# Kernel optimization log

Measured on AMD Instinct MI355X. Metric: run time of the kernel, lower is better.

The kernel has to match this reference:

```python
import jax, jax.numpy as jnp
import numpy as np

B, H, W = 16, 32, 64
HID, VOCAB, ENC_C, EMB = 256, 5000, 1024, 256


def _conv3x3(x, w, b):
    # x: [B,C,H,W], w: [O,I,3,3]
    y = jax.lax.conv_general_dilated(x, w, (1, 1), 'SAME',
                                     dimension_numbers=('NCHW', 'OIHW', 'NCHW'))
    return y + b[None, :, None, None]


def _gru(x, h, w_ih, w_hh, b_ih, b_hh):
    # torch GRUCell: gates ordered r, z, n
    gi = x @ w_ih.T + b_ih
    gh = h @ w_hh.T + b_hh
    ir, iz, inn = jnp.split(gi, 3, axis=1)
    hr, hz, hn = jnp.split(gh, 3, axis=1)
    r = jax.nn.sigmoid(ir + hr)
    z = jax.nn.sigmoid(iz + hz)
    n = jnp.tanh(inn + r * hn)
    return (1.0 - z) * n + z * h


def setup_inputs() -> dict:
    key = jax.random.key(0)
    ks = jax.random.split(key, 48)
    g = lambda i, shape, s=0.02: jax.random.normal(ks[i], shape, jnp.float32) * s
    inp = {
        'input_a': jax.random.randint(ks[0], (B,), 0, VOCAB),
        'input_hidden': jax.random.normal(ks[1], (B, 1, HID), jnp.float32),
        'encoder_outputs': jax.random.normal(ks[2], (B, ENC_C, H, W), jnp.float32),
        'attention_sum': jnp.zeros((B, 1, H, W), jnp.float32),
        'decoder_attention': jnp.zeros((B, 1, H, W), jnp.float32),
        'h_mask': jax.random.randint(ks[3], (B,), 1, H + 1),
        'w_mask': jax.random.randint(ks[4], (B,), 1, W + 1),
        'feature_w': W, 'feature_h': H, 'batch_size': B, 'gpu': 0,
        # parameters
        'emb_w': g(5, (VOCAB, EMB)),
        'gru1_w_ih': g(6, (3 * HID, EMB)), 'gru1_w_hh': g(7, (3 * HID, HID)),
        'gru1_b_ih': jnp.zeros((3 * HID,)), 'gru1_b_hh': jnp.zeros((3 * HID,)),
        'fc1_w': g(8, (256, HID)), 'fc1_b': jnp.zeros((256,)),
        'gru2_w_ih': g(9, (3 * HID, ENC_C)), 'gru2_w_hh': g(10, (3 * HID, HID)),
        'gru2_b_ih': jnp.zeros((3 * HID,)), 'gru2_b_hh': jnp.zeros((3 * HID,)),
        'out_w': g(11, (VOCAB, 128)), 'out_b': jnp.zeros((VOCAB,)),
        'emb2_w': g(12, (128, 256)), 'emb2_b': jnp.zeros((128,)),
        'conv1_w': g(13, (1, 1, 3, 3)), 'conv1_b': jnp.zeros((1,)),
        'convtan_w': g(14, (256, 256, 3, 3)), 'convtan_b': jnp.zeros((256,)),
        'fc2_w': g(15, (128, HID)), 'fc2_b': jnp.zeros((128,)),
        'ua_w': g(16, (256, ENC_C)), 'ua_b': jnp.zeros((256,)),
        'uf_w': g(17, (256, 1)), 'uf_b': jnp.zeros((256,)),
        'v_w': g(18, (1, 256)), 'v_b': jnp.zeros((1,)),
        'wc_w': g(19, (128, ENC_C)), 'wc_b': jnp.zeros((128,)),
        'bn1_g': jnp.ones((256,)), 'bn1_b': jnp.zeros((256,)),
        'bn1_rm': jnp.zeros((256,)), 'bn1_rv': jnp.ones((256,)),
    }
    return inp


def reference(input_a, input_hidden, encoder_outputs, feature_w, attention_sum,
              decoder_attention, feature_h, batch_size, h_mask, w_mask, gpu,
              emb_w, gru1_w_ih, gru1_w_hh, gru1_b_ih, gru1_b_hh, fc1_w, fc1_b,
              gru2_w_ih, gru2_w_hh, gru2_b_ih, gru2_b_hh, out_w, out_b,
              emb2_w, emb2_b, conv1_w, conv1_b, convtan_w, convtan_b,
              fc2_w, fc2_b, ua_w, ua_b, uf_w, uf_b, v_w, v_b, wc_w, wc_b,
              bn1_g, bn1_b, bn1_rm, bn1_rv):
    # vectorized mask construction (replaces per-batch python loop)
    mask = ((jnp.arange(feature_h)[None, :, None] < h_mask[:, None, None]) &
            (jnp.arange(feature_w)[None, None, :] < w_mask[:, None, None])
            ).astype(jnp.float32)  # [B,H,W]

    emb = emb_w[input_a]                                   # [B,256] (dropout=eval id)
    h0 = input_hidden.reshape(batch_size, HID)
    st = _gru(emb, h0, gru1_w_ih, gru1_w_hh, gru1_b_ih, gru1_b_hh)  # [B,HID]
    hidden1 = (st @ fc1_w.T + fc1_b)[:, None, None, :]     # [B,1,1,256]

    enc_t = jnp.transpose(encoder_outputs, (0, 2, 3, 1))   # [B,H,W,1024]
    dec_att = _conv3x3(decoder_attention, conv1_w, conv1_b)
    att_sum = attention_sum + dec_att                      # [B,1,H,W]
    att_t = jnp.transpose(att_sum, (0, 2, 3, 1))           # [B,H,W,1]

    enc1 = enc_t @ ua_w.T + ua_b                           # [B,H,W,256]
    att1 = att_t @ uf_w.T + uf_b                           # [B,H,W,256]
    et = hidden1 + enc1 + att1

    et_c = jnp.transpose(et, (0, 3, 1, 2))                 # [B,256,H,W]
    et_c = _conv3x3(et_c, convtan_w, convtan_b)
    et_c = et_c * mask[:, None]
    inv_std = (bn1_g / jnp.sqrt(bn1_rv + 1e-5))[None, :, None, None]
    et_c = (et_c - bn1_rm[None, :, None, None]) * inv_std + bn1_b[None, :, None, None]
    et_c = jnp.tanh(et_c)
    et_hw = jnp.transpose(et_c, (0, 2, 3, 1))              # [B,H,W,256]

    e = (et_hw @ v_w.T + v_b)[..., 0]                      # [B,H,W]
    e_exp = jnp.exp(e) * mask
    e_sum = e_exp.sum((1, 2))                              # [B]
    alpha = e_exp / (e_sum[:, None, None] + 1e-8)
    alpha4 = alpha[:, None]                                # [B,1,H,W]

    ct = (alpha4 * encoder_outputs).sum((2, 3))            # [B,1024]
    h2 = _gru(ct, st, gru2_w_ih, gru2_w_hh, gru2_b_ih, gru2_b_hh)
    hidden_next = h2[:, None, :]                           # [B,1,HID]

    pre = (h2 @ fc2_w.T + fc2_b) + (emb @ emb2_w.T + emb2_b) + (ct @ wc_w.T + wc_b)
    output = jax.nn.log_softmax(pre @ out_w.T + out_b, axis=1)[:, None, :]  # [B,1,V]
    return (output, hidden_next, alpha4, att_sum)
```

## Files before the change

kernel.cpp:

```cpp
#include <hip/hip_runtime.h>
#include <hip/hip_bf16.h>

#define HH 32
#define WW 64
#define HWSZ 2048
#define ENC 1024
#define VOCAB 5000

typedef __attribute__((ext_vector_type(8))) short short8;
typedef __attribute__((ext_vector_type(4))) short short4v;
typedef __attribute__((ext_vector_type(4))) float f32x4;

#if defined(__has_builtin)
#if __has_builtin(__builtin_amdgcn_global_load_lds)
#define HAVE_GLD_LDS 1
#endif
#endif

__device__ __forceinline__ float sigm(float x) { return 1.0f / (1.0f + expf(-x)); }

__device__ __forceinline__ unsigned short f2bf(float x) {
    unsigned u = __float_as_uint(x);
    unsigned r = (u + 0x7fff + ((u >> 16) & 1)) >> 16;
    return (unsigned short)r;
}

#ifdef HAVE_GLD_LDS
__device__ __forceinline__ void gld_lds16(const unsigned short* g, unsigned short* l) {
    __builtin_amdgcn_global_load_lds(
        (const __attribute__((address_space(1))) void*)g,
        (__attribute__((address_space(3))) void*)l,
        16, 0, 0);
}
#endif

template <int NI>
__device__ __forceinline__ float dotk(const float* __restrict__ w,
                                      const float* __restrict__ x, int l) {
    float s = 0.f;
    #pragma unroll
    for (int i = 0; i < NI; ++i) {
        f32x4 wv = *(const f32x4*)(w + i * 64 + l * 4);
        f32x4 xv = *(const f32x4*)(x + i * 64 + l * 4);
        s += wv.x * xv.x + wv.y * xv.y + wv.z * xv.z + wv.w * xv.w;
    }
    return s;
}
__device__ __forceinline__ float red16(float s) {
    s += __shfl_xor(s, 1, 64);
    s += __shfl_xor(s, 2, 64);
    s += __shfl_xor(s, 4, 64);
    s += __shfl_xor(s, 8, 64);
    return s;
}

__global__ __launch_bounds__(256) void k_prep(
    const float* __restrict__ ua_w, unsigned short* __restrict__ ub,
    const float* __restrict__ cw, unsigned short* __restrict__ wr,
    const float* __restrict__ att_in, const float* __restrict__ dec,
    const float* __restrict__ c1w, const float* __restrict__ c1b,
    float* __restrict__ out_attsum,
    const float* __restrict__ wb, const float* __restrict__ g,
    const float* __restrict__ bb, const float* __restrict__ rm,
    const float* __restrict__ rv, float* __restrict__ cs, float* __restrict__ csh,
    const int* __restrict__ input_a, const float* __restrict__ input_hidden,
    const float* __restrict__ emb_w,
    const float* __restrict__ w_ih, const float* __restrict__ w_hh,
    const float* __restrict__ b_ih, const float* __restrict__ b_hh,
    float* __restrict__ gi, float* __restrict__ gh,
    float* __restrict__ e_zero)
{
    int blk = blockIdx.x, t = threadIdx.x;
    if (blk < 1024) {
        int idx = blk * 256 + t;
        ub[idx] = f2bf(ua_w[idx]);
    } else if (blk < 1280) {
        int idx = (blk - 1024) * 256 + t;
        const float* p = cw + (size_t)idx * 9;
        #pragma unroll
        for (int k = 0; k < 9; ++k) wr[k * 65536 + idx] = f2bf(p[k]);
    } else if (blk < 1408) {
        int idx = (blk - 1280) * 256 + t;
        int b = idx >> 11, hw = idx & 2047;
        int h = hw >> 6, w = hw & 63;
        float s = c1b[0];
        #pragma unroll
        for (int dy = 0; dy < 3; ++dy) {
            int hh = h + dy - 1;
            if ((unsigned)hh < (unsigned)HH) {
                #pragma unroll
                for (int dx = 0; dx < 3; ++dx) {
                    int wi = w + dx - 1;
                    if ((unsigned)wi < (unsigned)WW)
                        s += dec[b * HWSZ + hh * WW + wi] * c1w[dy * 3 + dx];
                }
            }
        }
        out_attsum[idx] = att_in[idx] + s;
    } else if (blk == 1408) {
        int c = t;
        float s = g[c] * rsqrtf(rv[c] + 1e-5f);
        cs[c] = s;
        csh[c] = (wb[c] - rm[c]) * s + bb[c];
    } else if (blk < 2177) {
        int gid = (blk - 1409) * 256 + t;
        int o = gid >> 4, l = gid & 15;
        int j = o >> 4, b = o & 15;
        int ia = input_a[b];
        float si = dotk<4>(w_ih + (size_t)j * 256, emb_w + (size_t)ia * 256, l);
        float sh = dotk<4>(w_hh + (size_t)j * 256, input_hidden + b * 256, l);
        si = red16(si); sh = red16(sh);
        if (l == 0) {
            gi[j * 16 + b] = si + b_ih[j];
            gh[j * 16 + b] = sh + b_hh[j];
        }
    } else {
        e_zero[(blk - 2177) * 256 + t] = 0.f;
    }
}

__global__ __launch_bounds__(256) void k_frontbc(
    const int* __restrict__ input_a, const float* __restrict__ emb_w,
    const float* __restrict__ input_hidden,
    const float* __restrict__ gi, const float* __restrict__ gh,
    const float* __restrict__ fc1_w, const float* __restrict__ fc1_b,
    const float* __restrict__ ua_b, const float* __restrict__ uf_b,
    float* __restrict__ st, float* __restrict__ embv, float* __restrict__ addc)
{
    __shared__ float st_s[256];
    int b = blockIdx.x, i = threadIdx.x;
    float r = sigm(gi[i * 16 + b] + gh[i * 16 + b]);
    float z = sigm(gi[(256 + i) * 16 + b] + gh[(256 + i) * 16 + b]);
    float n = tanhf(gi[(512 + i) * 16 + b] + r * gh[(512 + i) * 16 + b]);
    float h0 = input_hidden[b * 256 + i];
    float v = (1.f - z) * n + z * h0;
    st_s[i] = v;
    st[b * 256 + i] = v;
    embv[b * 256 + i] = emb_w[(size_t)input_a[b] * 256 + i];
    __syncthreads();
    int c = i;
    const float* w = fc1_w + (size_t)c * 256;
    float acc = 0.f;
    for (int k = 0; k < 256; ++k) acc += st_s[k] * w[k];
    addc[b * 256 + c] = acc + fc1_b[c] + ua_b[c] + uf_b[c];
}

__global__ __launch_bounds__(256) void k_et(
    const float* __restrict__ enc, const unsigned short* __restrict__ ua_bf,
    const float* __restrict__ addc, const float* __restrict__ uf_w,
    const float* __restrict__ attsum, unsigned short* __restrict__ et)
{
    __shared__ __align__(16) unsigned short As[256 * 64];
    __shared__ __align__(16) unsigned short Bs[32 * 64];
    int t = threadIdx.x;
    int hw0 = blockIdx.x * 32, b = blockIdx.y;
    int wv = t >> 6;
    int l15 = t & 15, quad = (t >> 4) & 3;
    int xb = l15 & 7;
    f32x4 acc[4][2];
    #pragma unroll
    for (int i = 0; i < 4; ++i)
        #pragma unroll
        for (int j = 0; j < 2; ++j) acc[i][j] = (f32x4)0.f;

    int p = t & 31, g3 = t >> 5;
    const float* encb = enc + (size_t)b * ENC * HWSZ + hw0 + p;

    float pfv[8];
    {
        const float* ep = encb + (size_t)(g3 * 8) * HWSZ;
        #pragma unroll
        for (int j = 0; j < 8; ++j) pfv[j] = ep[(size_t)j * HWSZ];
    }

    for (int k0 = 0; k0 < ENC; k0 += 64) {
        short8 bv;
        #pragma unroll
        for (int j = 0; j < 8; ++j) bv[j] = (short)f2bf(pfv[j]);
        if (k0 + 64 < ENC) {
            const float* ep = encb + (size_t)(k0 + 64 + g3 * 8) * HWSZ;
            #pragma unroll
            for (int j = 0; j < 8; ++j) pfv[j] = ep[(size_t)j * HWSZ];
        }
        __syncthreads();

        #pragma unroll
        for (int i = 0; i < 8; ++i) {
            int s = t + 256 * i;
            int c = s >> 3, kq = s & 7;
            const unsigned short* src =
                ua_bf + (size_t)c * ENC + k0 + ((kq ^ (c & 7)) << 3);
#ifdef HAVE_GLD_LDS
            gld_lds16(src, As + (size_t)(wv * 64 + 256 * i) * 8);
#else
            *(uint4*)(As + (size_t)s * 8) = *(const uint4*)src;
#endif
        }
        *(short8*)(Bs + p * 64 + ((g3 ^ (p & 7)) << 3)) = bv;
        __syncthreads();

        #pragma unroll
        for (int kk = 0; kk < 2; ++kk) {
            short8 af[4], bfr[2];
            #pragma unroll
            for (int mt = 0; mt < 4; ++mt) {
                int c = wv * 64 + mt * 16 + l15;
                af[mt] = *(const short8*)(As + c * 64 + (((kk * 4 + quad) ^ xb) << 3));
            }
            #pragma unroll
            for (int nt = 0; nt < 2; ++nt) {
                int n = nt * 16 + l15;
                bfr[nt] = *(const short8*)(Bs + n * 64 + (((kk * 4 + quad) ^ xb) << 3));
            }
            #pragma unroll
            for (int mt = 0; mt < 4; ++mt)
                #pragma unroll
                for (int nt = 0; nt < 2; ++nt)
                    acc[mt][nt] = __builtin_amdgcn_mfma_f32_16x16x32_bf16(
                        af[mt], bfr[nt], acc[mt][nt], 0, 0, 0);
        }
    }
    float at[2];
    #pragma unroll
    for (int nt = 0; nt < 2; ++nt) at[nt] = attsum[b * HWSZ + hw0 + nt * 16 + l15];
    #pragma unroll
    for (int mt = 0; mt < 4; ++mt) {
        int cb = wv * 64 + mt * 16 + quad * 4;
        float ad[4], uw[4];
        #pragma unroll
        for (int r = 0; r < 4; ++r) { ad[r] = addc[b * 256 + cb + r]; uw[r] = uf_w[cb + r]; }
        #pragma unroll
        for (int nt = 0; nt < 2; ++nt) {
            ushort4 pk;
            pk.x = f2bf(acc[mt][nt][0] + ad[0] + at[nt] * uw[0]);
            pk.y = f2bf(acc[mt][nt][1] + ad[1] + at[nt] * uw[1]);
            pk.z = f2bf(acc[mt][nt][2] + ad[2] + at[nt] * uw[2]);
            pk.w = f2bf(acc[mt][nt][3] + ad[3] + at[nt] * uw[3]);
            *(ushort4*)(et + (size_t)(b * HWSZ + hw0 + nt * 16 + l15) * 256 + cb) = pk;
        }
    }
}

__global__ __launch_bounds__(256) void k_conv(
    const unsigned short* __restrict__ et, const unsigned short* __restrict__ wr,
    const float* __restrict__ cs, const float* __restrict__ csh,
    const float* __restrict__ v_w, float* __restrict__ e_out)
{
    __shared__ unsigned short Ls[66 * 264];
    __shared__ float red[64][17];
    int t = threadIdx.x;
    int h = blockIdx.x, c0 = blockIdx.y * 128, b = blockIdx.z;
    int wv = t >> 6, l15 = t & 15, quad = (t >> 4) & 3;
    f32x4 acc[2][4];
    #pragma unroll
    for (int i = 0; i < 2; ++i)
        #pragma unroll
        for (int j = 0; j < 4; ++j) acc[i][j] = (f32x4)0.f;

    for (int dy = 0; dy < 3; ++dy) {
        int hr = h + dy - 1;
        if ((unsigned)hr >= (unsigned)HH) continue;
        __syncthreads();
        const unsigned short* rowp = et + (size_t)(b * HH + hr) * WW * 256;
        for (int idx = t; idx < 2112; idx += 256) {
            int p = idx >> 5, s = idx & 31;
            short8 v;
            if (p == 0 || p == 65) v = (short8)0;
            else v = *(const short8*)(rowp + (p - 1) * 256 + s * 8);
            *(short8*)(Ls + p * 264 + s * 8) = v;
        }
        __syncthreads();
        for (int dx = 0; dx < 3; ++dx) {
            int tap = dy * 3 + dx;
            const unsigned short* wrt = wr + (size_t)tap * 65536;
            #pragma unroll
            for (int kc = 0; kc < 8; ++kc) {
                short8 af[2], bfr[4];
                #pragma unroll
                for (int mt = 0; mt < 2; ++mt)
                    af[mt] = *(const short8*)(wrt +
                        (size_t)(c0 + wv * 32 + mt * 16 + l15) * 256 + kc * 32 + quad * 8);
                #pragma unroll
                for (int nt = 0; nt < 4; ++nt) {
                    int wrow = nt * 16 + l15 + dx;
                    bfr[nt] = *(const short8*)(Ls + wrow * 264 + kc * 32 + quad * 8);
                }
                #pragma unroll
                for (int mt = 0; mt < 2; ++mt)
                    #pragma unroll
                    for (int nt = 0; nt < 4; ++nt)
                        acc[mt][nt] = __builtin_amdgcn_mfma_f32_16x16x32_bf16(
                            af[mt], bfr[nt], acc[mt][nt], 0, 0, 0);
            }
        }
    }
    float p[4] = {0.f, 0.f, 0.f, 0.f};
    #pragma unroll
    for (int mt = 0; mt < 2; ++mt) {
        int cb = c0 + wv * 32 + mt * 16 + quad * 4;
        #pragma unroll
        for (int r = 0; r < 4; ++r) {
            float sc = cs[cb + r], sh = csh[cb + r], vw = v_w[cb + r];
            #pragma unroll
            for (int nt = 0; nt < 4; ++nt) {
                float x = acc[mt][nt][r] * sc + sh;
                p[nt] += tanhf(x) * vw;
            }
        }
    }
    __syncthreads();
    #pragma unroll
    for (int nt = 0; nt < 4; ++nt) red[nt * 16 + l15][wv * 4 + quad] = p[nt];
    __syncthreads();
    if (t < 64) {
        float s = 0.f;
        #pragma unroll
        for (int i = 0; i < 16; ++i) s += red[t][i];
        atomicAdd(&e_out[(b * HH + h) * WW + t], s);
    }
}

__global__ __launch_bounds__(256) void k_ctalpha(
    const float* __restrict__ enc, const float* __restrict__ e_acc,
    const float* __restrict__ v_b,
    const int* __restrict__ h_mask, const int* __restrict__ w_mask,
    float* __restrict__ alpha_out, float* __restrict__ ct)
{
    __shared__ float a_s[HWSZ];
    __shared__ float rbuf[4];
    int b = blockIdx.y, cg = blockIdx.x, t = threadIdx.x;
    int hm = h_mask[b], wm = w_mask[b];
    float vb = v_b[0];
    float vals[8];
    float psum = 0.f;
    #pragma unroll
    for (int u = 0; u < 8; ++u) {
        int s = u * 256 + t;
        int h = s >> 6, w = s & 63;
        float e = e_acc[b * HWSZ + s] + vb;
        float ex = (h < hm && w < wm) ? expf(e) : 0.f;
        vals[u] = ex;
        psum += ex;
    }
    for (int off = 1; off < 64; off <<= 1) psum += __shfl_xor(psum, off, 64);
    if ((t & 63) == 0) rbuf[t >> 6] = psum;
    __syncthreads();
    float inv = 1.f / (rbuf[0] + rbuf[1] + rbuf[2] + rbuf[3] + 1e-8f);
    #pragma unroll
    for (int u = 0; u < 8; ++u) {
        int s = u * 256 + t;
        float a = vals[u] * inv;
        a_s[s] = a;
        if (cg == 0) alpha_out[b * HWSZ + s] = a;
    }
    __syncthreads();
    int wave = t >> 6, lane = t & 63;
    int c = cg * 4 + wave;
    const float* ep = enc + ((size_t)(b * ENC + c)) * HWSZ;
    float s = 0.f;
    for (int i = lane; i < HWSZ; i += 64) s += ep[i] * a_s[i];
    for (int off = 32; off; off >>= 1) s += __shfl_down(s, off, 64);
    if (lane == 0) ct[b * ENC + c] = s;
}

__global__ __launch_bounds__(256) void k_gru2a(
    const float* __restrict__ ct, const float* __restrict__ st,
    const float* __restrict__ w_ih, const float* __restrict__ w_hh,
    const float* __restrict__ b_ih, const float* __restrict__ b_hh,
    float* __restrict__ gi, float* __restrict__ gh)
{
    int gid = blockIdx.x * 256 + threadIdx.x;
    int o = gid >> 4, l = gid & 15;
    int j = o >> 4, b = o & 15;
    float si = dotk<16>(w_ih + (size_t)j * ENC, ct + b * ENC, l);
    float sh = dotk<4>(w_hh + (size_t)j * 256, st + b * 256, l);
    si = red16(si); sh = red16(sh);
    if (l == 0) {
        gi[j * 16 + b] = si + b_ih[j];
        gh[j * 16 + b] = sh + b_hh[j];
    }
}

__global__ __launch_bounds__(256) void k_gates2(
    const float* __restrict__ st, const float* __restrict__ gi,
    const float* __restrict__ gh, float* __restrict__ h2,
    float* __restrict__ out_hidden)
{
    int b = blockIdx.x, i = threadIdx.x;
    float r = sigm(gi[i * 16 + b] + gh[i * 16 + b]);
    float z = sigm(gi[(256 + i) * 16 + b] + gh[(256 + i) * 16 + b]);
    float n = tanhf(gi[(512 + i) * 16 + b] + r * gh[(512 + i) * 16 + b]);
    float v = (1.f - z) * n + z * st[b * 256 + i];
    h2[b * 256 + i] = v;
    out_hidden[b * 256 + i] = v;
}

__global__ __launch_bounds__(256) void k_pre(
    const float* __restrict__ h2, const float* __restrict__ emb,
    const float* __restrict__ ct,
    const float* __restrict__ fc2_w, const float* __restrict__ fc2_b,
    const float* __restrict__ emb2_w, const float* __restrict__ emb2_b,
    const float* __restrict__ wc_w, const float* __restrict__ wc_b,
    float* __restrict__ pre)
{
    int gid = blockIdx.x * 256 + threadIdx.x;
    int o = gid >> 4, l = gid & 15;
    int j = o >> 4, b = o & 15;
    float s = dotk<4>(fc2_w + (size_t)j * 256, h2 + b * 256, l)
            + dotk<4>(emb2_w + (size_t)j * 256, emb + b * 256, l)
            + dotk<16>(wc_w + (size_t)j * ENC, ct + b * ENC, l);
    s = red16(s);
    if (l == 0) pre[b * 128 + j] = s + fc2_b[j] + emb2_b[j] + wc_b[j];
}

__global__ __launch_bounds__(256) void k_logits(
    const float* __restrict__ pre, const float* __restrict__ out_w,
    const float* __restrict__ out_b, float* __restrict__ logits)
{
    int gid = blockIdx.x * 256 + threadIdx.x;
    int o = gid >> 4, l = gid & 15;
    int j = o >> 4, b = o & 15;
    float s = dotk<2>(out_w + (size_t)j * 128, pre + b * 128, l);
    s = red16(s);
    if (l == 0) logits[b * VOCAB + j] = s + out_b[j];
}

__global__ __launch_bounds__(256) void k_lsm(
    const float* __restrict__ logits, float* __restrict__ out)
{
    __shared__ float buf[VOCAB];
    __shared__ float rbuf[4];
    int b = blockIdx.x, t = threadIdx.x;
    float mx = -1e30f;
    for (int s = t; s < VOCAB; s += 256) {
        float v = logits[b * VOCAB + s];
        buf[s] = v;
        mx = fmaxf(mx, v);
    }
    for (int off = 1; off < 64; off <<= 1) mx = fmaxf(mx, __shfl_xor(mx, off, 64));
    if ((t & 63) == 0) rbuf[t >> 6] = mx;
    __syncthreads();
    mx = fmaxf(fmaxf(rbuf[0], rbuf[1]), fmaxf(rbuf[2], rbuf[3]));
    __syncthreads();
    float se = 0.f;
    for (int s = t; s < VOCAB; s += 256) se += expf(buf[s] - mx);
    for (int off = 1; off < 64; off <<= 1) se += __shfl_xor(se, off, 64);
    if ((t & 63) == 0) rbuf[t >> 6] = se;
    __syncthreads();
    float lse = mx + logf(rbuf[0] + rbuf[1] + rbuf[2] + rbuf[3]);
    for (int s = t; s < VOCAB; s += 256) out[b * VOCAB + s] = buf[s] - lse;
}

extern "C" void kernel_launch(void* const* d_in, const int* in_sizes, int n_in,
                              void* d_out, int out_size, void* d_ws, size_t ws_size,
                              hipStream_t stream)
{
    const int*   input_a      = (const int*)d_in[0];
    const float* input_hidden = (const float*)d_in[1];
    const float* enc          = (const float*)d_in[2];
    const float* att_in       = (const float*)d_in[3];
    const float* dec_att      = (const float*)d_in[4];
    const int*   h_mask       = (const int*)d_in[5];
    const int*   w_mask       = (const int*)d_in[6];
    const float* emb_w        = (const float*)d_in[11];
    const float* g1_wih       = (const float*)d_in[12];
    const float* g1_whh       = (const float*)d_in[13];
    const float* g1_bih       = (const float*)d_in[14];
    const float* g1_bhh       = (const float*)d_in[15];
    const float* fc1_w        = (const float*)d_in[16];
    const float* fc1_b        = (const float*)d_in[17];
    const float* g2_wih       = (const float*)d_in[18];
    const float* g2_whh       = (const float*)d_in[19];
    const float* g2_bih       = (const float*)d_in[20];
    const float* g2_bhh       = (const float*)d_in[21];
    const float* out_w        = (const float*)d_in[22];
    const float* out_b        = (const float*)d_in[23];
    const float* emb2_w       = (const float*)d_in[24];
    const float* emb2_b       = (const float*)d_in[25];
    const float* c1w          = (const float*)d_in[26];
    const float* c1b          = (const float*)d_in[27];
    const float* ctw          = (const float*)d_in[28];
    const float* ctb          = (const float*)d_in[29];
    const float* fc2_w        = (const float*)d_in[30];
    const float* fc2_b        = (const float*)d_in[31];
    const float* ua_w         = (const float*)d_in[32];
    const float* ua_b         = (const float*)d_in[33];
    const float* uf_w         = (const float*)d_in[34];
    const float* uf_b         = (const float*)d_in[35];
    const float* v_w          = (const float*)d_in[36];
    const float* v_b          = (const float*)d_in[37];
    const float* wc_w         = (const float*)d_in[38];
    const float* wc_b         = (const float*)d_in[39];
    const float* bn_g         = (const float*)d_in[40];
    const float* bn_b         = (const float*)d_in[41];
    const float* bn_rm        = (const float*)d_in[42];
    const float* bn_rv        = (const float*)d_in[43];

    float* out        = (float*)d_out;
    float* out_logits = out;
    float* out_hidden = out + 80000;
    float* out_alpha  = out + 84096;
    float* out_attsum = out + 116864;

    char* ws = (char*)d_ws;
    unsigned short* et_t  = (unsigned short*)ws;
    unsigned short* ua_bf = (unsigned short*)(ws + 16777216);
    unsigned short* w_r   = (unsigned short*)(ws + 17301504);
    float* f      = (float*)(ws + 18481152);
    float* st     = f;
    float* embv   = f + 4096;
    float* addc   = f + 8192;
    float* e_ws   = f + 12288;
    float* ct     = f + 45056;
    float* h2     = f + 61440;
    float* pre    = f + 65536;
    float* logits = f + 67584;
    float* gi1    = f + 147584;
    float* gh1    = f + 159872;
    float* gi2    = f + 172160;
    float* gh2    = f + 184448;
    float* cs     = f + 196736;
    float* csh    = f + 196992;

    k_prep<<<2305, 256, 0, stream>>>(ua_w, ua_bf, ctw, w_r,
                                     att_in, dec_att, c1w, c1b, out_attsum,
                                     ctb, bn_g, bn_b, bn_rm, bn_rv, cs, csh,
                                     input_a, input_hidden, emb_w,
                                     g1_wih, g1_whh, g1_bih, g1_bhh, gi1, gh1,
                                     e_ws);
    k_frontbc<<<16, 256, 0, stream>>>(input_a, emb_w, input_hidden, gi1, gh1,
                                      fc1_w, fc1_b, ua_b, uf_b, st, embv, addc);

    k_et<<<dim3(64, 16), 256, 0, stream>>>(enc, ua_bf, addc, uf_w, out_attsum, et_t);
    k_conv<<<dim3(32, 2, 16), 256, 0, stream>>>(et_t, w_r, cs, csh, v_w, e_ws);

    k_ctalpha<<<dim3(256, 16), 256, 0, stream>>>(enc, e_ws, v_b, h_mask, w_mask,
                                                 out_alpha, ct);
    k_gru2a<<<768, 256, 0, stream>>>(ct, st, g2_wih, g2_whh, g2_bih, g2_bhh, gi2, gh2);
    k_gates2<<<16, 256, 0, stream>>>(st, gi2, gh2, h2, out_hidden);
    k_pre<<<128, 256, 0, stream>>>(h2, embv, ct, fc2_w, fc2_b, emb2_w, emb2_b,
                                   wc_w, wc_b, pre);
    k_logits<<<5000, 256, 0, stream>>>(pre, out_w, out_b, logits);
    k_lsm<<<16, 256, 0, stream>>>(logits, out_logits);
}
```

Before: 452.0 us.

## Double-buffer conv input rows in LDS with async loads and XOR swizzle

Splits each 3x3 conv input row into two channel halves and stages them into double-buffered LDS using direct global-to-LDS loads, prefetching the next half-row while MFMAs consume the current one. The LDS layout switches from padded rows to an XOR swizzle, and a shared zero buffer stands in for the explicit border columns. It also adds an occupancy hint to launch bounds and raises wave priority around the MFMA section. The aim is to hide global load latency and cut LDS bank conflicts, at the cost of more syncs and extra address arithmetic.

```diff
diff --git a/kernel.cpp b/kernel.cpp
--- a/kernel.cpp
+++ b/kernel.cpp
@@ -241,13 +241,14 @@
     }
 }
 
-__global__ __launch_bounds__(256) void k_conv(
+__global__ __launch_bounds__(256, 4) void k_conv(
     const unsigned short* __restrict__ et, const unsigned short* __restrict__ wr,
     const float* __restrict__ cs, const float* __restrict__ csh,
     const float* __restrict__ v_w, float* __restrict__ e_out)
 {
-    __shared__ unsigned short Ls[66 * 264];
+    __shared__ __align__(16) unsigned short Lh[2 * 8192 + 128];
     __shared__ float red[64][17];
+    unsigned short* Zp = Lh + 16384;
     int t = threadIdx.x;
     int h = blockIdx.x, c0 = blockIdx.y * 128, b = blockIdx.z;
     int wv = t >> 6, l15 = t & 15, quad = (t >> 4) & 3;
@@ -257,33 +258,60 @@
         #pragma unroll
         for (int j = 0; j < 4; ++j) acc[i][j] = (f32x4)0.f;
 
-    for (int dy = 0; dy < 3; ++dy) {
-        int hr = h + dy - 1;
-        if ((unsigned)hr >= (unsigned)HH) continue;
-        __syncthreads();
-        const unsigned short* rowp = et + (size_t)(b * HH + hr) * WW * 256;
-        for (int idx = t; idx < 2112; idx += 256) {
-            int p = idx >> 5, s = idx & 31;
-            short8 v;
-            if (p == 0 || p == 65) v = (short8)0;
-            else v = *(const short8*)(rowp + (p - 1) * 256 + s * 8);
-            *(short8*)(Ls + p * 264 + s * 8) = v;
-        }
-        __syncthreads();
+    if (t < 16) *(short8*)(Zp + t * 8) = (short8)0;
+
+    int ni = 6, ibase = 0;
+    if (h == 0)           { ni = 4; ibase = 2; }
+    else if (h == HH - 1) { ni = 4; }
+
+    const unsigned short* etb = et + (size_t)b * HH * WW * 256;
+
+    auto stage = [&](int item, int bufsel) {
+        int dy = item >> 1, half = item & 1;
+        const unsigned short* rowp = etb + (size_t)(h + dy - 1) * WW * 256 + half * 128;
+        unsigned short* buf = Lh + bufsel * 8192;
+        #pragma unroll
+        for (int j = 0; j < 4; ++j) {
+            int s = t + 256 * j;
+            int r = s >> 4, o = s & 15;
+            const unsigned short* src = rowp + r * 256 + ((o ^ (r & 15)) << 3);
+#ifdef HAVE_GLD_LDS
+            gld_lds16(src, buf + (size_t)(wv * 64 + 256 * j) * 8);
+#else
+            *(uint4*)(buf + (size_t)s * 8) = *(const uint4*)src;
+#endif
+        }
+    };
+
+    stage(ibase, 0);
+    __syncthreads();
+
+    for (int i = 0; i < ni; ++i) {
+        if (i + 1 < ni) stage(ibase + i + 1, (i + 1) & 1);
+
+        int item = ibase + i;
+        int dy = item >> 1, half = item & 1;
+        const unsigned short* buf = Lh + (i & 1) * 8192;
+        __builtin_amdgcn_s_setprio(1);
+        #pragma unroll
         for (int dx = 0; dx < 3; ++dx) {
-            int tap = dy * 3 + dx;
-            const unsigned short* wrt = wr + (size_t)tap * 65536;
+            const unsigned short* wrt =
+                wr + (size_t)(dy * 3 + dx) * 65536 + half * 128;
             #pragma unroll
-            for (int kc = 0; kc < 8; ++kc) {
+            for (int kcl = 0; kcl < 4; ++kcl) {
                 short8 af[2], bfr[4];
                 #pragma unroll
                 for (int mt = 0; mt < 2; ++mt)
                     af[mt] = *(const short8*)(wrt +
-                        (size_t)(c0 + wv * 32 + mt * 16 + l15) * 256 + kc * 32 + quad * 8);
+                        (size_t)(c0 + wv * 32 + mt * 16 + l15) * 256 + kcl * 32 + quad * 8);
+                int o = kcl * 4 + quad;
                 #pragma unroll
                 for (int nt = 0; nt < 4; ++nt) {
-                    int wrow = nt * 16 + l15 + dx;
-                    bfr[nt] = *(const short8*)(Ls + wrow * 264 + kc * 32 + quad * 8);
+                    int r = nt * 16 + l15 + dx - 1;
+                    const unsigned short* p = ((unsigned)r < (unsigned)WW)
+                        ? buf + r * 128 + ((o ^ (r & 15)) << 3)
+                        : Zp + o * 8;
+                    bfr[nt] = *(const short8*)p;
                 }
                 #pragma unroll
                 for (int mt = 0; mt < 2; ++mt)
@@ -293,7 +321,10 @@
                             af[mt], bfr[nt], acc[mt][nt], 0, 0, 0);
             }
         }
-    }
+        __builtin_amdgcn_s_setprio(0);
+        __syncthreads();
+    }
+
     float p[4] = {0.f, 0.f, 0.f, 0.f};
     #pragma unroll
     for (int mt = 0; mt < 2; ++mt) {
```

Result: no change. 448.1 us (-0.9%).

## Double-buffer conv input rows and merge channel halves into one block

Applied to the files above, without the earlier changes.

The 3x3 conv kernel now computes all 256 output channels per block instead of splitting them across two blocks, so each input row is staged into LDS once rather than twice. The e-scores can then be written directly instead of accumulated with atomics. Input rows are prefetched into registers and written into a second LDS buffer while MFMAs run on the current one, with raised priority during the compute phase. The cost is twice as many accumulators per thread and half as many blocks (512), which reduces parallelism and puts pressure on registers. Since e_ws is still zeroed by the prep kernel, storing instead of adding gives the same values.

```diff
diff --git a/kernel.cpp b/kernel.cpp
--- a/kernel.cpp
+++ b/kernel.cpp
@@ -241,63 +241,94 @@
     }
 }
 
-__global__ __launch_bounds__(256) void k_conv(
+__global__ __launch_bounds__(256, 2) void k_conv(
     const unsigned short* __restrict__ et, const unsigned short* __restrict__ wr,
     const float* __restrict__ cs, const float* __restrict__ csh,
     const float* __restrict__ v_w, float* __restrict__ e_out)
 {
-    __shared__ unsigned short Ls[66 * 264];
+    __shared__ __align__(16) unsigned short Ls[2][66 * 264];
     __shared__ float red[64][17];
     int t = threadIdx.x;
-    int h = blockIdx.x, c0 = blockIdx.y * 128, b = blockIdx.z;
+    int h = blockIdx.x, b = blockIdx.y;
     int wv = t >> 6, l15 = t & 15, quad = (t >> 4) & 3;
-    f32x4 acc[2][4];
-    #pragma unroll
-    for (int i = 0; i < 2; ++i)
+    f32x4 acc[4][4];
+    #pragma unroll
+    for (int i = 0; i < 4; ++i)
         #pragma unroll
         for (int j = 0; j < 4; ++j) acc[i][j] = (f32x4)0.f;
 
-    for (int dy = 0; dy < 3; ++dy) {
-        int hr = h + dy - 1;
-        if ((unsigned)hr >= (unsigned)HH) continue;
-        __syncthreads();
-        const unsigned short* rowp = et + (size_t)(b * HH + hr) * WW * 256;
-        for (int idx = t; idx < 2112; idx += 256) {
-            int p = idx >> 5, s = idx & 31;
-            short8 v;
-            if (p == 0 || p == 65) v = (short8)0;
-            else v = *(const short8*)(rowp + (p - 1) * 256 + s * 8);
-            *(short8*)(Ls + p * 264 + s * 8) = v;
-        }
-        __syncthreads();
+    int ibase = (h == 0) ? 1 : 0;
+    int ni = (h == 0 || h == HH - 1) ? 2 : 3;
+    const unsigned short* etb = et + (size_t)b * HH * WW * 256;
+
+    uint4 sreg[9];
+    auto sload = [&](int dy) {
+        const unsigned short* rowp = etb + (size_t)(h + dy - 1) * WW * 256;
+        #pragma unroll
+        for (int j = 0; j < 9; ++j) {
+            int idx = t + 256 * j;
+            uint4 v = make_uint4(0u, 0u, 0u, 0u);
+            if (idx < 2112) {
+                int p = idx >> 5, s = idx & 31;
+                if (p > 0 && p < 65)
+                    v = *(const uint4*)(rowp + (p - 1) * 256 + s * 8);
+            }
+            sreg[j] = v;
+        }
+    };
+    auto swrite = [&](int bufsel) {
+        #pragma unroll
+        for (int j = 0; j < 9; ++j) {
+            int idx = t + 256 * j;
+            if (idx < 2112) {
+                int p = idx >> 5, s = idx & 31;
+                *(uint4*)(&Ls[bufsel][p * 264 + s * 8]) = sreg[j];
+            }
+        }
+    };
+
+    sload(ibase);
+    swrite(0);
+    __syncthreads();
+
+    for (int i = 0; i < ni; ++i) {
+        if (i + 1 < ni) sload(ibase + i + 1);
+        __builtin_amdgcn_sched_barrier(0);
+        int dy = ibase + i;
+        const unsigned short* L = &Ls[i & 1][0];
+        __builtin_amdgcn_s_setprio(1);
+        #pragma unroll
         for (int dx = 0; dx < 3; ++dx) {
-            int tap = dy * 3 + dx;
-            const unsigned short* wrt = wr + (size_t)tap * 65536;
+            const unsigned short* wrt = wr + (size_t)(dy * 3 + dx) * 65536;
             #pragma unroll
             for (int kc = 0; kc < 8; ++kc) {
-                short8 af[2], bfr[4];
+                short8 af[4], bfr[4];
                 #pragma unroll
-                for (int mt = 0; mt < 2; ++mt)
+                for (int mt = 0; mt < 4; ++mt)
                     af[mt] = *(const short8*)(wrt +
-                        (size_t)(c0 + wv * 32 + mt * 16 + l15) * 256 + kc * 32 + quad * 8);
+                        (size_t)(wv * 64 + mt * 16 + l15) * 256 + kc * 32 + quad * 8);
                 #pragma unroll
                 for (int nt = 0; nt < 4; ++nt) {
                     int wrow = nt * 16 + l15 + dx;
-                    bfr[nt] = *(const short8*)(Ls + wrow * 264 + kc * 32 + quad * 8);
+                    bfr[nt] = *(const short8*)(L + wrow * 264 + kc * 32 + quad * 8);
                 }
                 #pragma unroll
-                for (int mt = 0; mt < 2; ++mt)
+                for (int mt = 0; mt < 4; ++mt)
                     #pragma unroll
                     for (int nt = 0; nt < 4; ++nt)
                         acc[mt][nt] = __builtin_amdgcn_mfma_f32_16x16x32_bf16(
                             af[mt], bfr[nt], acc[mt][nt], 0, 0, 0);
             }
         }
-    }
+        __builtin_amdgcn_s_setprio(0);
+        if (i + 1 < ni) swrite((i + 1) & 1);
+        __syncthreads();
+    }
+
     float p[4] = {0.f, 0.f, 0.f, 0.f};
     #pragma unroll
-    for (int mt = 0; mt < 2; ++mt) {
-        int cb = c0 + wv * 32 + mt * 16 + quad * 4;
+    for (int mt = 0; mt < 4; ++mt) {
+        int cb = wv * 64 + mt * 16 + quad * 4;
         #pragma unroll
         for (int r = 0; r < 4; ++r) {
             float sc = cs[cb + r], sh = csh[cb + r], vw = v_w[cb + r];
@@ -308,7 +339,6 @@
             }
         }
     }
-    __syncthreads();
     #pragma unroll
     for (int nt = 0; nt < 4; ++nt) red[nt * 16 + l15][wv * 4 + quad] = p[nt];
     __syncthreads();
@@ -316,7 +346,7 @@
         float s = 0.f;
         #pragma unroll
         for (int i = 0; i < 16; ++i) s += red[t][i];
-        atomicAdd(&e_out[(b * HH + h) * WW + t], s);
+        e_out[(b * HH + h) * WW + t] = s;
     }
 }
 
@@ -532,7 +562,7 @@
                                       fc1_w, fc1_b, ua_b, uf_b, st, embv, addc);
 
     k_et<<<dim3(64, 16), 256, 0, stream>>>(enc, ua_bf, addc, uf_w, out_attsum, et_t);
-    k_conv<<<dim3(32, 2, 16), 256, 0, stream>>>(et_t, w_r, cs, csh, v_w, e_ws);
+    k_conv<<<dim3(32, 16), 256, 0, stream>>>(et_t, w_r, cs, csh, v_w, e_ws);
 
     k_ctalpha<<<dim3(256, 16), 256, 0, stream>>>(enc, e_ws, v_b, h_mask, w_mask,
                                                  out_alpha, ct);
```

Measured after the change: 459.7 us. No clear change (+1.7%).
